# Performance work log

Measured on AMD Instinct MI355X. Metric: run time of the kernel, lower is better.

## Reference

```python
import jax, jax.numpy as jnp
import numpy as np

WINDOW_SIZE = 11
SIGMA = 1.5
C1 = 0.01 ** 2
C2 = 0.03 ** 2


def _gaussian_window(channel, dtype):
    # 1D gaussian, normalized, then outer product -> 2D window [ws, ws]
    center = WINDOW_SIZE // 2
    x = jnp.arange(WINDOW_SIZE, dtype=jnp.float32) - center
    g = jnp.exp(-(x ** 2) / (2.0 * SIGMA ** 2))
    g = g / g.sum()
    w2d = jnp.outer(g, g)  # [ws, ws]
    # depthwise kernel: [C_out=channel, C_in/groups=1, ws, ws]
    return jnp.broadcast_to(w2d, (channel, 1, WINDOW_SIZE, WINDOW_SIZE)).astype(dtype)


def _depthwise_blur(x, window):
    pad = WINDOW_SIZE // 2
    return jax.lax.conv_general_dilated(
        x, window,
        window_strides=(1, 1),
        padding=[(pad, pad), (pad, pad)],
        feature_group_count=x.shape[1],
        dimension_numbers=('NCHW', 'OIHW', 'NCHW'))


def setup_inputs() -> dict:
    key = jax.random.key(0)
    k1, k2 = jax.random.split(key)
    img1 = jax.random.uniform(k1, (16, 3, 512, 512), dtype=jnp.float32)
    img2 = jax.random.uniform(k2, (16, 3, 512, 512), dtype=jnp.float32)
    return {"img1": img1, "img2": img2}


def reference(img1, img2):
    channel = img1.shape[1]
    window = _gaussian_window(channel, img1.dtype)

    mu1 = _depthwise_blur(img1, window)
    mu2 = _depthwise_blur(img2, window)
    mu1_sq = mu1 * mu1
    mu2_sq = mu2 * mu2
    mu1_mu2 = mu1 * mu2

    sigma1_sq = _depthwise_blur(img1 * img1, window) - mu1_sq
    sigma2_sq = _depthwise_blur(img2 * img2, window) - mu2_sq
    sigma12 = _depthwise_blur(img1 * img2, window) - mu1_mu2

    ssim_map = ((2.0 * mu1_mu2 + C1) * (2.0 * sigma12 + C2)) / (
        (mu1_sq + mu2_sq + C1) * (sigma1_sq + sigma2_sq + C2))
    return ssim_map.mean()  # size_average=True
```

## Files before the change

kernel.cpp:

```cpp
#include <hip/hip_runtime.h>


typedef _Float16 f16;
typedef __attribute__((ext_vector_type(4))) _Float16 f16x4;
typedef __attribute__((ext_vector_type(8))) _Float16 f16x8;
typedef __attribute__((ext_vector_type(4))) float f32x4;

#define IMGW 512
#define IMGH 512
#define NPL 48
#define NBX 8
#define NBY 8
#define NBLOCKS (NPL * NBX * NBY)
#define NPIX 12582912.0
#define REDT 1024

#define INV_T 0.99967202f

__device__ const float G_dev[11] = {0.00102838f, 0.00759876f, 0.03600077f,
                                    0.10936069f, 0.21300554f, 0.26601172f,
                                    0.21300554f, 0.10936069f, 0.03600077f,
                                    0.00759876f, 0.00102838f};

__global__ __launch_bounds__(256) void ssim_main(const float* __restrict__ img1,
                                                 const float* __restrict__ img2,
                                                 float* __restrict__ partial) {
    const int tid  = threadIdx.x;
    const int lane = tid & 63;
    const int wv   = tid >> 6;
    const int l15  = lane & 15;
    const int lg   = lane >> 4;

    const int bid   = blockIdx.x;
    const int plane = bid >> 6;
    const int rem   = bid & 63;
    const int by    = rem >> 3;
    const int bx    = rem & 7;
    const int r0    = by * 64 + wv * 16;
    const int c0    = bx * 64;

    const float* __restrict__ p1 = img1 + (size_t)plane * (IMGH * IMGW);
    const float* __restrict__ p2 = img2 + (size_t)plane * (IMGH * IMGW);

    int kap[8];
    #pragma unroll
    for (int j = 0; j < 8; ++j)
        kap[j] = (j < 4) ? (4 * lg + j) : (16 + 4 * lg + (j - 4));

    f16x8 bband;
    #pragma unroll
    for (int j = 0; j < 8; ++j) {
        const int t = kap[j] - l15;
        const float w = (t >= 0 && t < 11) ? G_dev[t] : 0.0f;
        bband[j] = (f16)w;
    }

    const f32x4 zero4 = {0.0f, 0.0f, 0.0f, 0.0f};

    f16x4 hv[5][5];
    #pragma unroll
    for (int t = 0; t < 5; ++t) {
        const int c   = c0 - 5 + 16 * t + l15;
        const bool cok = ((unsigned)c < (unsigned)IMGW);
        const int cc  = cok ? c : 0;
        float xv[8], yv[8];
        #pragma unroll
        for (int j = 0; j < 8; ++j) {
            const int rho = r0 - 5 + kap[j];
            const bool ok = cok && ((unsigned)rho < (unsigned)IMGH) && (kap[j] < 26);
            const int rc  = ((unsigned)rho < (unsigned)IMGH) ? rho : 0;
            const size_t off = (size_t)rc * IMGW + cc;
            const float a = p1[off];
            const float b = p2[off];
            xv[j] = ok ? a : 0.0f;
            yv[j] = ok ? b : 0.0f;
        }
        f16x8 fx, fy;
        #pragma unroll
        for (int j = 0; j < 8; ++j) {
            fx[j] = (f16)xv[j];
            fy[j] = (f16)yv[j];
        }
        const f16x8 fxx = fx * fx;
        const f16x8 fyy = fy * fy;
        const f16x8 fxy = fx * fy;

        const f32x4 dx  = __builtin_amdgcn_mfma_f32_16x16x32_f16(fx,  bband, zero4, 0, 0, 0);
        const f32x4 dy  = __builtin_amdgcn_mfma_f32_16x16x32_f16(fy,  bband, zero4, 0, 0, 0);
        const f32x4 dxx = __builtin_amdgcn_mfma_f32_16x16x32_f16(fxx, bband, zero4, 0, 0, 0);
        const f32x4 dyy = __builtin_amdgcn_mfma_f32_16x16x32_f16(fyy, bband, zero4, 0, 0, 0);
        const f32x4 dxy = __builtin_amdgcn_mfma_f32_16x16x32_f16(fxy, bband, zero4, 0, 0, 0);

        hv[t][0] = (f16x4){(f16)dx[0],  (f16)dx[1],  (f16)dx[2],  (f16)dx[3]};
        hv[t][1] = (f16x4){(f16)dy[0],  (f16)dy[1],  (f16)dy[2],  (f16)dy[3]};
        hv[t][2] = (f16x4){(f16)dxx[0], (f16)dxx[1], (f16)dxx[2], (f16)dxx[3]};
        hv[t][3] = (f16x4){(f16)dyy[0], (f16)dyy[1], (f16)dyy[2], (f16)dyy[3]};
        hv[t][4] = (f16x4){(f16)dxy[0], (f16)dxy[1], (f16)dxy[2], (f16)dxy[3]};
    }

    float acc = 0.0f;
    const float C1 = 1.0e-4f;
    const float C2 = 9.0e-4f;
    #pragma unroll
    for (int m = 0; m < 4; ++m) {
        f32x4 h[5];
        #pragma unroll
        for (int q = 0; q < 5; ++q) {
            const f16x8 a = __builtin_shufflevector(hv[m][q], hv[m + 1][q],
                                                    0, 1, 2, 3, 4, 5, 6, 7);
            h[q] = __builtin_amdgcn_mfma_f32_16x16x32_f16(a, bband, zero4, 0, 0, 0);
            h[q] *= INV_T;
        }
        #pragma unroll
        for (int r = 0; r < 4; ++r) {
            const float mu1 = h[0][r], mu2 = h[1][r];
            const float exx = h[2][r], eyy = h[3][r], exy = h[4][r];
            const float mu1s = mu1 * mu1;
            const float mu2s = mu2 * mu2;
            const float mu12 = mu1 * mu2;
            const float s1  = exx - mu1s;
            const float s2  = eyy - mu2s;
            const float s12 = exy - mu12;
            const float num = fmaf(2.0f, mu12, C1) * fmaf(2.0f, s12, C2);
            const float den = (mu1s + mu2s + C1) * (s1 + s2 + C2);
            float rd = __builtin_amdgcn_rcpf(den);
            rd = rd * fmaf(-den, rd, 2.0f);
            acc = fmaf(num, rd, acc);
        }
    }

    #pragma unroll
    for (int off = 32; off > 0; off >>= 1)
        acc += __shfl_down(acc, off, 64);
    __shared__ float wsum[4];
    if (lane == 0) wsum[wv] = acc;
    __syncthreads();
    if (tid == 0)
        partial[bid] = (wsum[0] + wsum[1]) + (wsum[2] + wsum[3]);
}

__global__ __launch_bounds__(REDT) void ssim_reduce(const float* __restrict__ partial,
                                                    float* __restrict__ out) {
    const int tid = threadIdx.x;
    double s = 0.0;
    for (int i = tid; i < NBLOCKS; i += REDT)
        s += (double)partial[i];
    #pragma unroll
    for (int off = 32; off > 0; off >>= 1)
        s += __shfl_down(s, off, 64);
    __shared__ double wsd[REDT / 64];
    if ((tid & 63) == 0) wsd[tid >> 6] = s;
    __syncthreads();
    if (tid == 0) {
        double t = 0.0;
        #pragma unroll
        for (int i = 0; i < REDT / 64; ++i) t += wsd[i];
        out[0] = (float)(t / NPIX);
    }
}

extern "C" void kernel_launch(void* const* d_in, const int* in_sizes, int n_in,
                              void* d_out, int out_size, void* d_ws, size_t ws_size,
                              hipStream_t stream) {
    const float* img1 = (const float*)d_in[0];
    const float* img2 = (const float*)d_in[1];
    float* partial = (float*)d_ws;
    float* out = (float*)d_out;
    ssim_main<<<NBLOCKS, 256, 0, stream>>>(img1, img2, partial);
    ssim_reduce<<<1, REDT, 0, stream>>>(partial, out);
}
```

Measured before the change: 46.36 us.

## Stage shared input tile in LDS as fp16 to reuse halo across waves

The block now cooperatively loads an 80-row by 80-column halo tile of both images once, converts it to fp16, and stores it column-major in shared memory. Each wave then reads its MFMA operands from LDS instead of issuing its own strided global loads. Previously the four waves fetched overlapping row windows, so this removes redundant global traffic. Interior blocks skip the bounds checks entirely. It adds a barrier, about 27KB of LDS per block and an occupancy hint of 4 blocks per CU, which may limit residency.

```diff
diff --git a/kernel.cpp b/kernel.cpp
--- a/kernel.cpp
+++ b/kernel.cpp
@@ -9,11 +9,13 @@
 #define IMGW 512
 #define IMGH 512
 #define NPL 48
-#define NBX 8
-#define NBY 8
-#define NBLOCKS (NPL * NBX * NBY)
+#define NBLOCKS (NPL * 8 * 8)
 #define NPIX 12582912.0
 #define REDT 1024
+
+#define SR 84
+#define NC 80
+#define IMGOFF (NC * SR)
 
 #define INV_T 0.99967202f
 
@@ -22,9 +24,49 @@
                                     0.21300554f, 0.10936069f, 0.03600077f,
                                     0.00759876f, 0.00102838f};
 
-__global__ __launch_bounds__(256) void ssim_main(const float* __restrict__ img1,
-                                                 const float* __restrict__ img2,
-                                                 float* __restrict__ partial) {
+template<bool EDGE>
+__device__ __forceinline__ void stage(const float* __restrict__ p1,
+                                      const float* __restrict__ p2,
+                                      int R0, int AC0, int tid, f16* sT) {
+    #pragma unroll
+    for (int it = 0; it < 13; ++it) {
+        const int idx = tid + it * 256;
+        if (it == 12 && idx >= 3200) break;
+        const int img  = (idx >= 1600) ? 1 : 0;
+        const int rem  = idx - img * 1600;
+        const int g    = rem / NC;
+        const int lcol = rem - g * NC;
+        const float* __restrict__ base = img ? p2 : p1;
+        const int gc = AC0 + lcol;
+        const int gr = R0 + 4 * g;
+        float v[4];
+        if (EDGE) {
+            const bool cok = ((unsigned)gc < (unsigned)IMGW);
+            const int cc = cok ? gc : 0;
+            #pragma unroll
+            for (int e = 0; e < 4; ++e) {
+                const int r  = gr + e;
+                const bool ok = cok && ((unsigned)r < (unsigned)IMGH);
+                const int rc = (r < 0) ? 0 : (r > IMGH - 1 ? IMGH - 1 : r);
+                const float x = base[(size_t)rc * IMGW + cc];
+                v[e] = ok ? x : 0.0f;
+            }
+        } else {
+            #pragma unroll
+            for (int e = 0; e < 4; ++e)
+                v[e] = base[(size_t)(gr + e) * IMGW + gc];
+        }
+        const f16x4 h = {(f16)v[0], (f16)v[1], (f16)v[2], (f16)v[3]};
+        *(f16x4*)&sT[(size_t)img * IMGOFF + (size_t)lcol * SR + 4 * g] = h;
+    }
+}
+
+__global__ __launch_bounds__(256, 4) void ssim_main(const float* __restrict__ img1,
+                                                    const float* __restrict__ img2,
+                                                    float* __restrict__ partial) {
+    __shared__ f16 sT[2 * IMGOFF];
+    __shared__ float wsum[4];
+
     const int tid  = threadIdx.x;
     const int lane = tid & 63;
     const int wv   = tid >> 6;
@@ -36,21 +78,25 @@
     const int rem   = bid & 63;
     const int by    = rem >> 3;
     const int bx    = rem & 7;
-    const int r0    = by * 64 + wv * 16;
+    const int r0b   = by * 64;
     const int c0    = bx * 64;
+    const int R0    = r0b - 5;
+    const int AC0   = c0 - 8;
 
     const float* __restrict__ p1 = img1 + (size_t)plane * (IMGH * IMGW);
     const float* __restrict__ p2 = img2 + (size_t)plane * (IMGH * IMGW);
 
-    int kap[8];
-    #pragma unroll
-    for (int j = 0; j < 8; ++j)
-        kap[j] = (j < 4) ? (4 * lg + j) : (16 + 4 * lg + (j - 4));
+    if (by >= 1 && by <= 6 && bx >= 1 && bx <= 6)
+        stage<false>(p1, p2, R0, AC0, tid, sT);
+    else
+        stage<true >(p1, p2, R0, AC0, tid, sT);
+    __syncthreads();
 
     f16x8 bband;
     #pragma unroll
     for (int j = 0; j < 8; ++j) {
-        const int t = kap[j] - l15;
+        const int kj = (j < 4) ? (4 * lg + j) : (16 + 4 * lg + (j - 4));
+        const int t  = kj - l15;
         const float w = (t >= 0 && t < 11) ? G_dev[t] : 0.0f;
         bband[j] = (f16)w;
     }
@@ -60,27 +106,17 @@
     f16x4 hv[5][5];
     #pragma unroll
     for (int t = 0; t < 5; ++t) {
-        const int c   = c0 - 5 + 16 * t + l15;
-        const bool cok = ((unsigned)c < (unsigned)IMGW);
-        const int cc  = cok ? c : 0;
-        float xv[8], yv[8];
-        #pragma unroll
-        for (int j = 0; j < 8; ++j) {
-            const int rho = r0 - 5 + kap[j];
-            const bool ok = cok && ((unsigned)rho < (unsigned)IMGH) && (kap[j] < 26);
-            const int rc  = ((unsigned)rho < (unsigned)IMGH) ? rho : 0;
-            const size_t off = (size_t)rc * IMGW + cc;
-            const float a = p1[off];
-            const float b = p2[off];
-            xv[j] = ok ? a : 0.0f;
-            yv[j] = ok ? b : 0.0f;
-        }
-        f16x8 fx, fy;
-        #pragma unroll
-        for (int j = 0; j < 8; ++j) {
-            fx[j] = (f16)xv[j];
-            fy[j] = (f16)yv[j];
-        }
+        int col = 3 + 16 * t + l15;
+        if (t == 4) col = (col > NC - 1) ? NC - 1 : col;
+        const int ro = 16 * wv + 4 * lg;
+        const f16* __restrict__ cb1 = sT + (size_t)col * SR;
+        const f16* __restrict__ cb2 = sT + IMGOFF + (size_t)col * SR;
+        const f16x4 xlo = *(const f16x4*)&cb1[ro];
+        const f16x4 xhi = *(const f16x4*)&cb1[ro + 16];
+        const f16x4 ylo = *(const f16x4*)&cb2[ro];
+        const f16x4 yhi = *(const f16x4*)&cb2[ro + 16];
+        const f16x8 fx = __builtin_shufflevector(xlo, xhi, 0, 1, 2, 3, 4, 5, 6, 7);
+        const f16x8 fy = __builtin_shufflevector(ylo, yhi, 0, 1, 2, 3, 4, 5, 6, 7);
         const f16x8 fxx = fx * fx;
         const f16x8 fyy = fy * fy;
         const f16x8 fxy = fx * fy;
@@ -132,7 +168,6 @@
     #pragma unroll
     for (int off = 32; off > 0; off >>= 1)
         acc += __shfl_down(acc, off, 64);
-    __shared__ float wsum[4];
     if (lane == 0) wsum[wv] = acc;
     __syncthreads();
     if (tid == 0)
```

After: 50.48 us. +8.9%, slower.

## Stage image tiles in LDS via direct global-to-LDS loads before MFMA blur

Applied to the files above, without the earlier changes.

Each block now cooperatively copies a haloed 74x80 tile of both images into shared memory using global_load_lds 16-byte transfers, with zero-fill for edge blocks and the padding rows. The per-lane scattered global loads of the previous version are replaced by LDS reads, removing the redundant halo refetches across waves. Launch bounds now request 3 blocks per CU. The change adds about 54KB of LDS per block and extra synchronization, which limits occupancy.

```diff
diff --git a/kernel.cpp b/kernel.cpp
--- a/kernel.cpp
+++ b/kernel.cpp
@@ -9,11 +9,13 @@
 #define IMGW 512
 #define IMGH 512
 #define NPL 48
-#define NBX 8
-#define NBY 8
-#define NBLOCKS (NPL * NBX * NBY)
+#define NBLOCKS (NPL * 8 * 8)
 #define NPIX 12582912.0
 #define REDT 1024
+
+#define SRW 84
+#define PROWS 80
+#define IMGOFFD (PROWS * SRW)
 
 #define INV_T 0.99967202f
 
@@ -22,9 +24,12 @@
                                     0.21300554f, 0.10936069f, 0.03600077f,
                                     0.00759876f, 0.00102838f};
 
-__global__ __launch_bounds__(256) void ssim_main(const float* __restrict__ img1,
-                                                 const float* __restrict__ img2,
-                                                 float* __restrict__ partial) {
+__global__ __launch_bounds__(256, 3) void ssim_main(const float* __restrict__ img1,
+                                                    const float* __restrict__ img2,
+                                                    float* __restrict__ partial) {
+    __shared__ __align__(16) float sP[2 * IMGOFFD];
+    __shared__ float wsum[4];
+
     const int tid  = threadIdx.x;
     const int lane = tid & 63;
     const int wv   = tid >> 6;
@@ -36,21 +41,57 @@
     const int rem   = bid & 63;
     const int by    = rem >> 3;
     const int bx    = rem & 7;
-    const int r0    = by * 64 + wv * 16;
-    const int c0    = bx * 64;
+    const int R0    = by * 64 - 5;
+    const int AC0   = bx * 64 - 8;
 
     const float* __restrict__ p1 = img1 + (size_t)plane * (IMGH * IMGW);
     const float* __restrict__ p2 = img2 + (size_t)plane * (IMGH * IMGW);
 
-    int kap[8];
-    #pragma unroll
-    for (int j = 0; j < 8; ++j)
-        kap[j] = (j < 4) ? (4 * lg + j) : (16 + 4 * lg + (j - 4));
+    const int rlo = (R0 < 0) ? -R0 : 0;
+    const int rhi = (R0 + 74 > IMGH) ? (IMGH - R0) : 74;
+    const int llo = (AC0 < 0) ? ((-AC0 + 3) >> 2) : 0;
+    const int lhic = (IMGW - AC0) >> 2;
+    const int lhi = (lhic < 20) ? lhic : 20;
+    const bool edge = (rlo != 0) | (rhi != 74) | (llo != 0) | (lhi != 20);
+
+    if (edge) {
+        for (int it = 0; it < 27; ++it) {
+            const int i = tid + it * 256;
+            if (i < 6720) *(float2*)&sP[2 * i] = make_float2(0.0f, 0.0f);
+        }
+        __syncthreads();
+    } else {
+        #pragma unroll
+        for (int it = 0; it < 2; ++it) {
+            const int i = tid + it * 256;
+            if (i < 504) {
+                const int im = (i >= 252) ? 1 : 0;
+                const int k  = i - im * 252;
+                *(float2*)&sP[im * IMGOFFD + 74 * SRW + 2 * k] = make_float2(0.0f, 0.0f);
+            }
+        }
+    }
+
+    {
+        const int nr = rhi - rlo;
+        for (int L = wv; L < 2 * nr; L += 4) {
+            const int im  = (L >= nr) ? 1 : 0;
+            const int row = rlo + (L - im * nr);
+            const float* __restrict__ bp = im ? p2 : p1;
+            float* lp = &sP[im * IMGOFFD + row * SRW];
+            if (lane >= llo && lane < lhi) {
+                const float* gp = bp + (size_t)(R0 + row) * IMGW + (AC0 + 4 * lane);
+                __builtin_amdgcn_global_load_lds(gp, lp, 16, 0, 0);
+            }
+        }
+    }
+    __syncthreads();
 
     f16x8 bband;
     #pragma unroll
     for (int j = 0; j < 8; ++j) {
-        const int t = kap[j] - l15;
+        const int kj = (j < 4) ? (4 * lg + j) : (16 + 4 * lg + (j - 4));
+        const int t  = kj - l15;
         const float w = (t >= 0 && t < 11) ? G_dev[t] : 0.0f;
         bband[j] = (f16)w;
     }
@@ -60,26 +101,18 @@
     f16x4 hv[5][5];
     #pragma unroll
     for (int t = 0; t < 5; ++t) {
-        const int c   = c0 - 5 + 16 * t + l15;
-        const bool cok = ((unsigned)c < (unsigned)IMGW);
-        const int cc  = cok ? c : 0;
-        float xv[8], yv[8];
-        #pragma unroll
-        for (int j = 0; j < 8; ++j) {
-            const int rho = r0 - 5 + kap[j];
-            const bool ok = cok && ((unsigned)rho < (unsigned)IMGH) && (kap[j] < 26);
-            const int rc  = ((unsigned)rho < (unsigned)IMGH) ? rho : 0;
-            const size_t off = (size_t)rc * IMGW + cc;
-            const float a = p1[off];
-            const float b = p2[off];
-            xv[j] = ok ? a : 0.0f;
-            yv[j] = ok ? b : 0.0f;
-        }
+        int p = 3 + 16 * t + l15;
+        if (t == 4) p = (p > PROWS - 1) ? PROWS - 1 : p;
+        const int ro = 16 * wv + 4 * lg;
+        const float* __restrict__ b1 = &sP[ro * SRW + p];
+        const float* __restrict__ b2 = &sP[IMGOFFD + ro * SRW + p];
         f16x8 fx, fy;
         #pragma unroll
-        for (int j = 0; j < 8; ++j) {
-            fx[j] = (f16)xv[j];
-            fy[j] = (f16)yv[j];
+        for (int e = 0; e < 4; ++e) {
+            fx[e]     = (f16)b1[e * SRW];
+            fx[e + 4] = (f16)b1[(16 + e) * SRW];
+            fy[e]     = (f16)b2[e * SRW];
+            fy[e + 4] = (f16)b2[(16 + e) * SRW];
         }
         const f16x8 fxx = fx * fx;
         const f16x8 fyy = fy * fy;
@@ -132,7 +165,6 @@
     #pragma unroll
     for (int off = 32; off > 0; off >>= 1)
         acc += __shfl_down(acc, off, 64);
-    __shared__ float wsum[4];
     if (lane == 0) wsum[wv] = acc;
     __syncthreads();
     if (tid == 0)
```

Result: slower. 57.01 us (+23.0%).
